# Kernel tuning notes

Hardware: AMD Instinct MI355X
Metric: run time of the kernel (lower is better)

The kernel has to match this reference:

```python
import jax, jax.numpy as jnp
import numpy as np

B, IN_CAPS, IN_DIM = 64, 2048, 16
NUM_CAPS, DIM_CAPS = 32, 16
NUM_ROUTING = 3
EPS = 1e-7


def squash(s):
    # squash along last (capsule vector) dim: ||s||^2/(1+||s||^2) * s/||s||
    sq_norm = jnp.sum(s * s, axis=-1, keepdims=True)
    scale = sq_norm / (1.0 + sq_norm) / jnp.sqrt(sq_norm + EPS)
    return scale * s


def setup_inputs() -> dict:
    key = jax.random.key(0)
    k1, k2 = jax.random.split(key)
    inputs = jax.random.normal(k1, (B, IN_CAPS, IN_DIM), dtype=jnp.float32)
    # original code inits xavier then overwrites with uniform(-1, 1)
    W = jax.random.uniform(k2, (IN_CAPS, NUM_CAPS, IN_DIM, DIM_CAPS),
                           dtype=jnp.float32, minval=-1.0, maxval=1.0)
    return {"inputs": inputs, "W": W}


def reference(inputs, W):
    # inputs_hat: [b, i(in_caps), j(num_caps), m(dim_caps)]
    inputs_hat = jnp.einsum('ijnm,bin->bijm', W, inputs)
    b = jnp.zeros((inputs.shape[0], IN_CAPS, NUM_CAPS), dtype=inputs.dtype)
    outputs = None
    for i in range(NUM_ROUTING):
        c = jax.nn.softmax(b, axis=1)                      # over input capsules
        outputs = squash(jnp.einsum('bij,bijm->bjm', c, inputs_hat))
        if i < NUM_ROUTING - 1:
            b = b + jnp.einsum('bjm,bijm->bij', outputs, inputs_hat)
    return outputs
```

## Files before the change

### kernel.cpp

```cpp
#include <hip/hip_runtime.h>
#include <hip/hip_fp16.h>
#include <math.h>

#define BATCH    64
#define IN_CAPS  2048
#define IN_DIM   16
#define NUM_CAPS 32
#define DIM_CAPS 16
#define NROUTE   3
#define CAPS_EPS 1e-7f

typedef unsigned short ushort_t;

__global__ __launch_bounds__(256) void caps_hat_kernel(
    const float* __restrict__ x, const float* __restrict__ W,
    ushort_t* __restrict__ hat)
{
  const int bid   = blockIdx.x;
  const int ig    = bid & 127;
  const int jb    = bid >> 7;
  const int bhalf = blockIdx.y;
  const int t     = threadIdx.x;
  const int wv    = t >> 6;
  const int l     = t & 63;
  const int j     = jb * 4 + wv;
  const int i_loc = l >> 2;
  const int m0    = (l & 3) * 4;
  const int i     = ig * 16 + i_loc;

  float4 Wr[16];
  {
    const float* wbase = W + (((size_t)i * NUM_CAPS + j) * IN_DIM) * DIM_CAPS + m0;
#pragma unroll
    for (int n = 0; n < 16; ++n)
      Wr[n] = *reinterpret_cast<const float4*>(wbase + n * DIM_CAPS);
  }

  __shared__ float xs[16][16][20];

  for (int bc = 0; bc < 2; ++bc) {
    const int b0 = bhalf * 32 + bc * 16;
#pragma unroll
    for (int k = 0; k < 4; ++k) {
      const int u   = t + k * 256;
      const int bl  = u >> 6;
      const int rem = u & 63;
      const int il  = rem >> 2;
      const int n0  = (rem & 3) * 4;
      float4 v = *reinterpret_cast<const float4*>(
          x + ((size_t)(b0 + bl) * IN_CAPS + ig * 16 + il) * IN_DIM + n0);
      *reinterpret_cast<float4*>(&xs[bl][il][n0]) = v;
    }
    __syncthreads();
#pragma unroll
    for (int bl = 0; bl < 16; ++bl) {
      const int b = b0 + bl;
      float4 acc = make_float4(0.f, 0.f, 0.f, 0.f);
#pragma unroll
      for (int nb = 0; nb < 4; ++nb) {
        const float4 xv = *reinterpret_cast<const float4*>(&xs[bl][i_loc][nb * 4]);
        acc.x = fmaf(Wr[4 * nb + 0].x, xv.x, acc.x);
        acc.y = fmaf(Wr[4 * nb + 0].y, xv.x, acc.y);
        acc.z = fmaf(Wr[4 * nb + 0].z, xv.x, acc.z);
        acc.w = fmaf(Wr[4 * nb + 0].w, xv.x, acc.w);
        acc.x = fmaf(Wr[4 * nb + 1].x, xv.y, acc.x);
        acc.y = fmaf(Wr[4 * nb + 1].y, xv.y, acc.y);
        acc.z = fmaf(Wr[4 * nb + 1].z, xv.y, acc.z);
        acc.w = fmaf(Wr[4 * nb + 1].w, xv.y, acc.w);
        acc.x = fmaf(Wr[4 * nb + 2].x, xv.z, acc.x);
        acc.y = fmaf(Wr[4 * nb + 2].y, xv.z, acc.y);
        acc.z = fmaf(Wr[4 * nb + 2].z, xv.z, acc.z);
        acc.w = fmaf(Wr[4 * nb + 2].w, xv.z, acc.w);
        acc.x = fmaf(Wr[4 * nb + 3].x, xv.w, acc.x);
        acc.y = fmaf(Wr[4 * nb + 3].y, xv.w, acc.y);
        acc.z = fmaf(Wr[4 * nb + 3].z, xv.w, acc.z);
        acc.w = fmaf(Wr[4 * nb + 3].w, xv.w, acc.w);
      }
      ushort4 st;
      st.x = __half_as_ushort(__float2half(acc.x));
      st.y = __half_as_ushort(__float2half(acc.y));
      st.z = __half_as_ushort(__float2half(acc.z));
      st.w = __half_as_ushort(__float2half(acc.w));
      *reinterpret_cast<ushort4*>(
          hat + (((size_t)b * NUM_CAPS + j) * IN_CAPS + i) * DIM_CAPS + m0) = st;
    }
    __syncthreads();
  }
}

__global__ __launch_bounds__(512) void caps_route_kernel(
    const ushort_t* __restrict__ hat, float* __restrict__ out)
{
  __shared__ float red[8][20];
  __shared__ float outs[16];

  const int bid  = blockIdx.x;
  const int t    = threadIdx.x;
  const int lane = t & 63;
  const int wv   = t >> 6;
  const int mh   = t & 1;

  const ushort_t* base = hat + (size_t)bid * (IN_CAPS * DIM_CAPS);

  uint4 g[8];
#pragma unroll
  for (int q = 0; q < 8; ++q)
    g[q] = *reinterpret_cast<const uint4*>(base + (size_t)(t + 512 * q) * 8);

#define HVAL(q, s) __half2float(__ushort_as_half((ushort_t)( \
    ((s) & 1) ? (((const unsigned int*)&g[(q)])[(s) >> 1] >> 16) \
              : (((const unsigned int*)&g[(q)])[(s) >> 1] & 0xffffu))))

  const int b1 = (lane >> 1) & 1;
  const int b2 = (lane >> 2) & 1;
  const int b3 = (lane >> 3) & 1;
  const int m_fin = 8 * mh + 4 * b3 + 2 * b2 + b1;

  float lg[8];
#pragma unroll
  for (int q = 0; q < 8; ++q) lg[q] = 0.f;

  for (int r = 0; r < NROUTE; ++r) {
    float e[8];
    float Ep = 0.f;
    if (r == 0) {
#pragma unroll
      for (int q = 0; q < 8; ++q) e[q] = 1.f;
    } else {
#pragma unroll
      for (int q = 0; q < 8; ++q) { e[q] = __expf(lg[q]); Ep += e[q]; }
    }

    float acc[8];
#pragma unroll
    for (int s = 0; s < 8; ++s) {
      float a = 0.f;
#pragma unroll
      for (int q = 0; q < 8; ++q) a = fmaf(e[q], HVAL(q, s), a);
      acc[s] = a;
    }

    float v4[4];
#pragma unroll
    for (int k = 0; k < 4; ++k) {
      float send = b1 ? acc[2 * k] : acc[2 * k + 1];
      float recv = __shfl_xor(send, 2);
      float keep = b1 ? acc[2 * k + 1] : acc[2 * k];
      v4[k] = keep + recv;
    }
    float v2[2];
#pragma unroll
    for (int k = 0; k < 2; ++k) {
      float send = b2 ? v4[2 * k] : v4[2 * k + 1];
      float recv = __shfl_xor(send, 4);
      float keep = b2 ? v4[2 * k + 1] : v4[2 * k];
      v2[k] = keep + recv;
    }
    float z;
    {
      float send = b3 ? v2[0] : v2[1];
      float recv = __shfl_xor(send, 8);
      float keep = b3 ? v2[1] : v2[0];
      z = keep + recv;
    }
    z += __shfl_xor(z, 16);
    z += __shfl_xor(z, 32);

    if (r > 0) {
      Ep += __shfl_xor(Ep, 2);
      Ep += __shfl_xor(Ep, 4);
      Ep += __shfl_xor(Ep, 8);
      Ep += __shfl_xor(Ep, 16);
      Ep += __shfl_xor(Ep, 32);
      if (lane == 16) red[wv][16] = Ep;
    }
    if (lane < 16) red[wv][m_fin] = z;
    __syncthreads();

    if (t < 16) {
      float s = 0.f;
#pragma unroll
      for (int w = 0; w < 8; ++w) s += red[w][t];
      float E;
      if (r == 0) E = (float)IN_CAPS;
      else {
        E = 0.f;
#pragma unroll
        for (int w = 0; w < 8; ++w) E += red[w][16];
      }
      float sm = s / E;
      float n2 = sm * sm;
#pragma unroll
      for (int off = 8; off >= 1; off >>= 1) n2 += __shfl_xor(n2, off);
      const float scale = n2 / (1.0f + n2) * rsqrtf(n2 + CAPS_EPS);
      const float o = scale * sm;
      outs[t] = o;
      if (r == NROUTE - 1)
        out[(size_t)bid * DIM_CAPS + t] = o;
    }
    __syncthreads();

    if (r < NROUTE - 1) {
#pragma unroll
      for (int q = 0; q < 8; ++q) {
        float d = 0.f;
#pragma unroll
        for (int s = 0; s < 8; ++s) d = fmaf(outs[8 * mh + s], HVAL(q, s), d);
        d += __shfl_xor(d, 1);
        lg[q] += d;
      }
    }
  }
#undef HVAL
}

extern "C" void kernel_launch(void* const* d_in, const int* in_sizes, int n_in,
                              void* d_out, int out_size, void* d_ws, size_t ws_size,
                              hipStream_t stream) {
  (void)in_sizes; (void)n_in; (void)out_size; (void)ws_size;
  const float* x = (const float*)d_in[0];
  const float* W = (const float*)d_in[1];
  float* outp = (float*)d_out;
  ushort_t* hat = (ushort_t*)d_ws;

  caps_hat_kernel<<<dim3(1024, 2), dim3(256), 0, stream>>>(x, W, hat);
  caps_route_kernel<<<dim3(BATCH * NUM_CAPS), dim3(512), 0, stream>>>(hat, outp);
}
```

Measured before the change: 85.38 us.

## Drop LDS staging in hat kernel; loop full batch with register-prefetched x rows

The hat kernel no longer stages x tiles in shared memory with barriers. Each thread instead reads its own x row straight from global memory, prefetching the next batch row into registers while computing the current one. The grid is halved so each block covers all 64 batches, which amortizes the W register load over twice as many batches. In exchange there are fewer blocks, and several lanes issue redundant global x loads (four lanes share each row), relying on the cache.

```diff
diff --git a/kernel.cpp b/kernel.cpp
--- a/kernel.cpp
+++ b/kernel.cpp
@@ -19,7 +19,6 @@
   const int bid   = blockIdx.x;
   const int ig    = bid & 127;
   const int jb    = bid >> 7;
-  const int bhalf = blockIdx.y;
   const int t     = threadIdx.x;
   const int wv    = t >> 6;
   const int l     = t & 63;
@@ -36,55 +35,50 @@
       Wr[n] = *reinterpret_cast<const float4*>(wbase + n * DIM_CAPS);
   }
 
-  __shared__ float xs[16][16][20];
-
-  for (int bc = 0; bc < 2; ++bc) {
-    const int b0 = bhalf * 32 + bc * 16;
-#pragma unroll
-    for (int k = 0; k < 4; ++k) {
-      const int u   = t + k * 256;
-      const int bl  = u >> 6;
-      const int rem = u & 63;
-      const int il  = rem >> 2;
-      const int n0  = (rem & 3) * 4;
-      float4 v = *reinterpret_cast<const float4*>(
-          x + ((size_t)(b0 + bl) * IN_CAPS + ig * 16 + il) * IN_DIM + n0);
-      *reinterpret_cast<float4*>(&xs[bl][il][n0]) = v;
-    }
-    __syncthreads();
-#pragma unroll
-    for (int bl = 0; bl < 16; ++bl) {
-      const int b = b0 + bl;
-      float4 acc = make_float4(0.f, 0.f, 0.f, 0.f);
-#pragma unroll
-      for (int nb = 0; nb < 4; ++nb) {
-        const float4 xv = *reinterpret_cast<const float4*>(&xs[bl][i_loc][nb * 4]);
-        acc.x = fmaf(Wr[4 * nb + 0].x, xv.x, acc.x);
-        acc.y = fmaf(Wr[4 * nb + 0].y, xv.x, acc.y);
-        acc.z = fmaf(Wr[4 * nb + 0].z, xv.x, acc.z);
-        acc.w = fmaf(Wr[4 * nb + 0].w, xv.x, acc.w);
-        acc.x = fmaf(Wr[4 * nb + 1].x, xv.y, acc.x);
-        acc.y = fmaf(Wr[4 * nb + 1].y, xv.y, acc.y);
-        acc.z = fmaf(Wr[4 * nb + 1].z, xv.y, acc.z);
-        acc.w = fmaf(Wr[4 * nb + 1].w, xv.y, acc.w);
-        acc.x = fmaf(Wr[4 * nb + 2].x, xv.z, acc.x);
-        acc.y = fmaf(Wr[4 * nb + 2].y, xv.z, acc.y);
-        acc.z = fmaf(Wr[4 * nb + 2].z, xv.z, acc.z);
-        acc.w = fmaf(Wr[4 * nb + 2].w, xv.z, acc.w);
-        acc.x = fmaf(Wr[4 * nb + 3].x, xv.w, acc.x);
-        acc.y = fmaf(Wr[4 * nb + 3].y, xv.w, acc.y);
-        acc.z = fmaf(Wr[4 * nb + 3].z, xv.w, acc.z);
-        acc.w = fmaf(Wr[4 * nb + 3].w, xv.w, acc.w);
-      }
-      ushort4 st;
-      st.x = __half_as_ushort(__float2half(acc.x));
-      st.y = __half_as_ushort(__float2half(acc.y));
-      st.z = __half_as_ushort(__float2half(acc.z));
-      st.w = __half_as_ushort(__float2half(acc.w));
-      *reinterpret_cast<ushort4*>(
-          hat + (((size_t)b * NUM_CAPS + j) * IN_CAPS + i) * DIM_CAPS + m0) = st;
-    }
-    __syncthreads();
+  const float* xrow = x + (size_t)i * IN_DIM;
+  ushort_t* hbase = hat + (((size_t)j * IN_CAPS + i) * DIM_CAPS + m0);
+
+  float4 xb[4], xn[4];
+#pragma unroll
+  for (int k = 0; k < 4; ++k)
+    xb[k] = *reinterpret_cast<const float4*>(xrow + 4 * k);
+
+  for (int b = 0; b < BATCH; ++b) {
+    if (b + 1 < BATCH) {
+      const float* xr = xrow + (size_t)(b + 1) * (IN_CAPS * IN_DIM);
+#pragma unroll
+      for (int k = 0; k < 4; ++k)
+        xn[k] = *reinterpret_cast<const float4*>(xr + 4 * k);
+    }
+    float4 acc = make_float4(0.f, 0.f, 0.f, 0.f);
+#pragma unroll
+    for (int nb = 0; nb < 4; ++nb) {
+      const float4 xv = xb[nb];
+      acc.x = fmaf(Wr[4 * nb + 0].x, xv.x, acc.x);
+      acc.y = fmaf(Wr[4 * nb + 0].y, xv.x, acc.y);
+      acc.z = fmaf(Wr[4 * nb + 0].z, xv.x, acc.z);
+      acc.w = fmaf(Wr[4 * nb + 0].w, xv.x, acc.w);
+      acc.x = fmaf(Wr[4 * nb + 1].x, xv.y, acc.x);
+      acc.y = fmaf(Wr[4 * nb + 1].y, xv.y, acc.y);
+      acc.z = fmaf(Wr[4 * nb + 1].z, xv.y, acc.z);
+      acc.w = fmaf(Wr[4 * nb + 1].w, xv.y, acc.w);
+      acc.x = fmaf(Wr[4 * nb + 2].x, xv.z, acc.x);
+      acc.y = fmaf(Wr[4 * nb + 2].y, xv.z, acc.y);
+      acc.z = fmaf(Wr[4 * nb + 2].z, xv.z, acc.z);
+      acc.w = fmaf(Wr[4 * nb + 2].w, xv.z, acc.w);
+      acc.x = fmaf(Wr[4 * nb + 3].x, xv.w, acc.x);
+      acc.y = fmaf(Wr[4 * nb + 3].y, xv.w, acc.y);
+      acc.z = fmaf(Wr[4 * nb + 3].z, xv.w, acc.z);
+      acc.w = fmaf(Wr[4 * nb + 3].w, xv.w, acc.w);
+    }
+    ushort4 st;
+    st.x = __half_as_ushort(__float2half(acc.x));
+    st.y = __half_as_ushort(__float2half(acc.y));
+    st.z = __half_as_ushort(__float2half(acc.z));
+    st.w = __half_as_ushort(__float2half(acc.w));
+    *reinterpret_cast<ushort4*>(hbase + (size_t)b * (NUM_CAPS * IN_CAPS * DIM_CAPS)) = st;
+#pragma unroll
+    for (int k = 0; k < 4; ++k) xb[k] = xn[k];
   }
 }
 
@@ -223,6 +217,6 @@
   float* outp = (float*)d_out;
   ushort_t* hat = (ushort_t*)d_ws;
 
-  caps_hat_kernel<<<dim3(1024, 2), dim3(256), 0, stream>>>(x, W, hat);
+  caps_hat_kernel<<<dim3(1024), dim3(256), 0, stream>>>(x, W, hat);
   caps_route_kernel<<<dim3(BATCH * NUM_CAPS), dim3(512), 0, stream>>>(hat, outp);
 }
```

After: 113.1 us. 32.4% more time.
